# Kernel tuning notes

Measured on AMD Instinct MI355X. Metric: run time of the kernel, lower is better.

Reference implementation:

```python
import jax, jax.numpy as jnp
import numpy as np

N_NODES = 50000
N_EDGES = 800000
IN_DIM, HID_DIM, OUT_DIM = 128, 256, 64


def setup_inputs() -> dict:
    key = jax.random.key(0)
    k1, k2, k3, k4 = jax.random.split(key, 4)
    x = jax.random.normal(k1, (N_NODES, IN_DIM), dtype=jnp.float32)
    edge_index = jax.random.randint(k2, (2, N_EDGES), 0, N_NODES, dtype=jnp.int32)
    # Glorot-ish scaled weights
    W1 = jax.random.normal(k3, (IN_DIM, HID_DIM), dtype=jnp.float32) * (1.0 / np.sqrt(IN_DIM))
    W2 = jax.random.normal(k4, (HID_DIM, OUT_DIM), dtype=jnp.float32) * (1.0 / np.sqrt(HID_DIM))
    b1 = jnp.zeros((HID_DIM,), dtype=jnp.float32)
    b2 = jnp.zeros((OUT_DIM,), dtype=jnp.float32)
    return {"x": x, "edge_index": edge_index, "W1": W1, "b1": b1, "W2": W2, "b2": b2}


def _gcn_conv(x, src, dst, deg_inv_sqrt, W, b):
    # transform first (PyG GCNConv order), then edge-normalized scatter-add
    h = x @ W                                        # [N, D_out]
    norm = deg_inv_sqrt[src] * deg_inv_sqrt[dst]     # [E]
    msgs = h[src] * norm[:, None]                    # [E, D_out]
    agg = jax.ops.segment_sum(msgs, dst, num_segments=x.shape[0])
    return agg + b


def reference(x, edge_index, W1, b1, W2, b2):
    n = x.shape[0]
    loops = jnp.arange(n, dtype=edge_index.dtype)
    src = jnp.concatenate([edge_index[0], loops])    # add self-loops
    dst = jnp.concatenate([edge_index[1], loops])
    deg = jax.ops.segment_sum(jnp.ones_like(dst, dtype=x.dtype), dst, num_segments=n)
    deg_inv_sqrt = jnp.where(deg > 0, jax.lax.rsqrt(jnp.maximum(deg, 1e-12)), 0.0)
    h = jax.nn.relu(_gcn_conv(x, src, dst, deg_inv_sqrt, W1, b1))
    h = _gcn_conv(h, src, dst, deg_inv_sqrt, W2, b2)
    return jax.nn.log_softmax(h, axis=1)
```

## Files before the change

kernel.cpp:

```cpp
#include <hip/hip_runtime.h>
#include <hip/hip_bf16.h>
#include <math.h>

#define N_NODES 50000
#define N_EDGES 800000
#define IN_DIM 128
#define HID_DIM 256
#define OUT_DIM 64
#define NPART 196
#define CAP 8192
#define CHUNK 2048
#define NPB ((N_EDGES + CHUNK - 1) / CHUNK)

typedef __attribute__((ext_vector_type(8))) short bf16x8;
typedef __attribute__((ext_vector_type(4))) short short4v;
typedef __attribute__((ext_vector_type(4))) float f32x4;

__device__ inline short f2bf(float f) {
    unsigned u = __float_as_uint(f);
    unsigned r = (u + 0x7fffu + ((u >> 16) & 1u)) >> 16;
    return (short)r;
}
__device__ inline float bf_lo(unsigned u) { return __uint_as_float(u << 16); }
__device__ inline float bf_hi(unsigned u) { return __uint_as_float(u & 0xffff0000u); }

__global__ __launch_bounds__(256) void part1_pack_kernel(const int* __restrict__ src,
                                                         const int* __restrict__ dst,
                                                         int* __restrict__ coarseCursor,
                                                         uint2* __restrict__ sedge,
                                                         const float* __restrict__ W1,
                                                         const float* __restrict__ W2,
                                                         short* __restrict__ Bp1,
                                                         short* __restrict__ Bp2, int E) {
    __shared__ int cnt_l[NPART];
    __shared__ int pref[NPART];
    __shared__ int gbase[NPART];
    __shared__ int ws4[4];
    __shared__ uint2 stage[CHUNK];
    int tid = threadIdx.x;
    if (blockIdx.x >= NPB) {
        int idx = (blockIdx.x - NPB) * 256 + tid;
        const float* W; short* Bp; int N;
        const int T1 = (IN_DIM / 32) * (HID_DIM / 16) * 64;
        const int T2 = (HID_DIM / 32) * (OUT_DIM / 16) * 64;
        if (idx < T1) { W = W1; Bp = Bp1; N = HID_DIM; }
        else { idx -= T1; if (idx >= T2) return; W = W2; Bp = Bp2; N = OUT_DIM; }
        int lane = idx & 63;
        int frag = idx >> 6;
        int ntiles = N >> 4;
        int nt = frag % ntiles;
        int kt = frag / ntiles;
        int col = nt * 16 + (lane & 15);
        int krow = kt * 32 + (lane >> 4) * 8;
        bf16x8 pk;
        #pragma unroll
        for (int j = 0; j < 8; j++) pk[j] = f2bf(W[(size_t)(krow + j) * N + col]);
        *((bf16x8*)(Bp + (size_t)idx * 8)) = pk;
        return;
    }
    int e0 = blockIdx.x * CHUNK;
    if (tid < NPART) cnt_l[tid] = 0;
    __syncthreads();
    int es[CHUNK / 256], ed[CHUNK / 256];
    #pragma unroll
    for (int j = 0; j < CHUNK / 256; j++) {
        int e = e0 + j * 256 + tid;
        if (e < E) {
            es[j] = src[e]; ed[j] = dst[e];
            atomicAdd(&cnt_l[ed[j] >> 8], 1);
        } else ed[j] = -1;
    }
    __syncthreads();
    int lane = tid & 63, wid = tid >> 6;
    int v = (tid < NPART) ? cnt_l[tid] : 0;
    int s = v;
    #pragma unroll
    for (int off = 1; off < 64; off <<= 1) {
        int t = __shfl_up(s, off, 64);
        if (lane >= off) s += t;
    }
    if (lane == 63) ws4[wid] = s;
    __syncthreads();
    int wp = 0;
    #pragma unroll
    for (int w = 0; w < 4; w++) wp += (w < wid) ? ws4[w] : 0;
    int excl = s - v + wp;
    if (tid < NPART) pref[tid] = excl;
    __syncthreads();
    if (tid < NPART) cnt_l[tid] = excl;
    __syncthreads();
    #pragma unroll
    for (int j = 0; j < CHUNK / 256; j++) {
        if (ed[j] >= 0) {
            int c = ed[j] >> 8;
            int p = atomicAdd(&cnt_l[c], 1);
            stage[p] = make_uint2((unsigned)es[j], (unsigned)ed[j]);
        }
    }
    __syncthreads();
    if (tid < NPART) {
        int cl = cnt_l[tid] - pref[tid];
        gbase[tid] = (cl > 0) ? (tid * CAP + atomicAdd(&coarseCursor[tid], cl)) : 0;
    }
    __syncthreads();
    int total = (e0 + CHUNK <= E) ? CHUNK : (E - e0);
    for (int i = tid; i < total; i += 256) {
        uint2 ev = stage[i];
        int c = (int)(ev.y >> 8);
        sedge[gbase[c] + (i - pref[c])] = ev;
    }
}

__global__ __launch_bounds__(256) void part2_kernel(const uint2* __restrict__ sedge,
                                                    const int* __restrict__ coarseCnt,
                                                    int* __restrict__ offs,
                                                    int* __restrict__ cntg,
                                                    float* __restrict__ dis,
                                                    int* __restrict__ ssrc,
                                                    const float* __restrict__ x,
                                                    short* __restrict__ xb, int n) {
    __shared__ int kcnt[256];
    __shared__ int ws4[4];
    __shared__ float sdis[256];
    int b = blockIdx.x, tid = threadIdx.x;
    int base = b * CAP;
    int cb = coarseCnt[b];
    kcnt[tid] = 0;
    __syncthreads();
    for (int i = tid; i < cb; i += 256) {
        uint2 ev = sedge[base + i];
        atomicAdd(&kcnt[ev.y & 255], 1);
    }
    __syncthreads();
    int v = kcnt[tid];
    int lane = tid & 63, wid = tid >> 6;
    int s = v;
    #pragma unroll
    for (int off = 1; off < 64; off <<= 1) {
        int t = __shfl_up(s, off, 64);
        if (lane >= off) s += t;
    }
    if (lane == 63) ws4[wid] = s;
    __syncthreads();
    int wp = 0;
    #pragma unroll
    for (int w = 0; w < 4; w++) wp += (w < wid) ? ws4[w] : 0;
    int excl = s - v + wp;
    int node = b * 256 + tid;
    float dn = rsqrtf((float)v + 1.0f);
    if (node < n) {
        offs[node] = base + excl;
        cntg[node] = v;
        dis[node] = dn;
    }
    sdis[tid] = dn;
    __syncthreads();
    kcnt[tid] = base + excl;
    __syncthreads();
    for (int i = tid; i < cb; i += 256) {
        uint2 ev = sedge[base + i];
        int pos = atomicAdd(&kcnt[ev.y & 255], 1);
        ssrc[pos] = (int)ev.x;
    }
    int rlane = tid & 31, rgrp = tid >> 5;
    for (int rb = 0; rb < 32; rb++) {
        int row = rb * 8 + rgrp;
        int nd = b * 256 + row;
        if (nd >= n) break;
        float d2 = sdis[row];
        float4 vv = ((const float4*)(x + (size_t)nd * IN_DIM))[rlane];
        short4v o = {f2bf(vv.x * d2), f2bf(vv.y * d2), f2bf(vv.z * d2), f2bf(vv.w * d2)};
        *((short4v*)(xb + (size_t)nd * IN_DIM + rlane * 4)) = o;
    }
}

__global__ void agg1_kernel(const short* __restrict__ xb, const int* __restrict__ ssrc,
                            const int* __restrict__ offs, const int* __restrict__ cnt,
                            const float* __restrict__ dis, short* __restrict__ aggx, int n) {
    int lane = threadIdx.x & 63;
    int node = blockIdx.x * 4 + (threadIdx.x >> 6);
    if (node >= n) return;
    int grp = lane >> 3, l8 = lane & 7;
    int start = offs[node], c = cnt[node];
    int vidx = (lane < c) ? ssrc[start + lane] : 0;
    float acc[16] = {};
    int lim = (c < 64) ? c : 64;
    int rounds = (lim + 15) >> 4;
    for (int r = 0; r < rounds; r++) {
        int j0 = r * 16 + grp;
        int j1 = j0 + 8;
        int i0 = (j0 < 63) ? j0 : 63;
        int i1 = (j1 < 63) ? j1 : 63;
        int s0 = __shfl(vidx, i0, 64);
        int s1 = __shfl(vidx, i1, 64);
        float g0 = (j0 < lim) ? 1.0f : 0.0f;
        float g1 = (j1 < lim) ? 1.0f : 0.0f;
        const uint4* r0 = (const uint4*)(xb + (size_t)s0 * IN_DIM + l8 * 16);
        const uint4* r1 = (const uint4*)(xb + (size_t)s1 * IN_DIM + l8 * 16);
        uint4 a0 = r0[0], a1 = r0[1];
        uint4 b0 = r1[0], b1 = r1[1];
        acc[0]  += g0 * bf_lo(a0.x); acc[1]  += g0 * bf_hi(a0.x);
        acc[2]  += g0 * bf_lo(a0.y); acc[3]  += g0 * bf_hi(a0.y);
        acc[4]  += g0 * bf_lo(a0.z); acc[5]  += g0 * bf_hi(a0.z);
        acc[6]  += g0 * bf_lo(a0.w); acc[7]  += g0 * bf_hi(a0.w);
        acc[8]  += g0 * bf_lo(a1.x); acc[9]  += g0 * bf_hi(a1.x);
        acc[10] += g0 * bf_lo(a1.y); acc[11] += g0 * bf_hi(a1.y);
        acc[12] += g0 * bf_lo(a1.z); acc[13] += g0 * bf_hi(a1.z);
        acc[14] += g0 * bf_lo(a1.w); acc[15] += g0 * bf_hi(a1.w);
        acc[0]  += g1 * bf_lo(b0.x); acc[1]  += g1 * bf_hi(b0.x);
        acc[2]  += g1 * bf_lo(b0.y); acc[3]  += g1 * bf_hi(b0.y);
        acc[4]  += g1 * bf_lo(b0.z); acc[5]  += g1 * bf_hi(b0.z);
        acc[6]  += g1 * bf_lo(b0.w); acc[7]  += g1 * bf_hi(b0.w);
        acc[8]  += g1 * bf_lo(b1.x); acc[9]  += g1 * bf_hi(b1.x);
        acc[10] += g1 * bf_lo(b1.y); acc[11] += g1 * bf_hi(b1.y);
        acc[12] += g1 * bf_lo(b1.z); acc[13] += g1 * bf_hi(b1.z);
        acc[14] += g1 * bf_lo(b1.w); acc[15] += g1 * bf_hi(b1.w);
    }
    for (int j = 64 + grp; j < c; j += 8) {
        int s0 = ssrc[start + j];
        const uint4* r0 = (const uint4*)(xb + (size_t)s0 * IN_DIM + l8 * 16);
        uint4 a0 = r0[0], a1 = r0[1];
        acc[0]  += bf_lo(a0.x); acc[1]  += bf_hi(a0.x); acc[2]  += bf_lo(a0.y); acc[3]  += bf_hi(a0.y);
        acc[4]  += bf_lo(a0.z); acc[5]  += bf_hi(a0.z); acc[6]  += bf_lo(a0.w); acc[7]  += bf_hi(a0.w);
        acc[8]  += bf_lo(a1.x); acc[9]  += bf_hi(a1.x); acc[10] += bf_lo(a1.y); acc[11] += bf_hi(a1.y);
        acc[12] += bf_lo(a1.z); acc[13] += bf_hi(a1.z); acc[14] += bf_lo(a1.w); acc[15] += bf_hi(a1.w);
    }
    #pragma unroll
    for (int k = 0; k < 16; k++) {
        acc[k] += __shfl_xor(acc[k], 8, 64);
        acc[k] += __shfl_xor(acc[k], 16, 64);
        acc[k] += __shfl_xor(acc[k], 32, 64);
    }
    if (grp == 0) {
        float dn = dis[node];
        const uint4* rs = (const uint4*)(xb + (size_t)node * IN_DIM + l8 * 16);
        uint4 a0 = rs[0], a1 = rs[1];
        acc[0]  += bf_lo(a0.x); acc[1]  += bf_hi(a0.x); acc[2]  += bf_lo(a0.y); acc[3]  += bf_hi(a0.y);
        acc[4]  += bf_lo(a0.z); acc[5]  += bf_hi(a0.z); acc[6]  += bf_lo(a0.w); acc[7]  += bf_hi(a0.w);
        acc[8]  += bf_lo(a1.x); acc[9]  += bf_hi(a1.x); acc[10] += bf_lo(a1.y); acc[11] += bf_hi(a1.y);
        acc[12] += bf_lo(a1.z); acc[13] += bf_hi(a1.z); acc[14] += bf_lo(a1.w); acc[15] += bf_hi(a1.w);
        bf16x8 o0, o1;
        #pragma unroll
        for (int k = 0; k < 8; k++) { o0[k] = f2bf(acc[k] * dn); o1[k] = f2bf(acc[k + 8] * dn); }
        short* dst0 = aggx + (size_t)node * IN_DIM + l8 * 16;
        *((bf16x8*)dst0) = o0;
        *((bf16x8*)(dst0 + 8)) = o1;
    }
}

#define H1_STRIDE 264
__global__ __launch_bounds__(256) void gemm_fused_kernel(const short* __restrict__ A,
                                                         const short* __restrict__ Bp1,
                                                         const short* __restrict__ Bp2,
                                                         const float* __restrict__ b1,
                                                         const float* __restrict__ dis,
                                                         short* __restrict__ h2, int M) {
    __shared__ short lds_h1[4][16][H1_STRIDE];
    int lane = threadIdx.x & 63;
    int w = threadIdx.x >> 6;
    int rowBase = blockIdx.x * 64 + w * 16;
    int arow = rowBase + (lane & 15);
    int kseg = lane >> 4;
    int col0 = lane & 15;

    constexpr int NT1 = HID_DIM / 16;
    f32x4 acc1[NT1] = {};
    #pragma unroll
    for (int kt = 0; kt < IN_DIM / 32; kt++) {
        bf16x8 a = {};
        if (arow < M)
            a = *((const bf16x8*)(A + (size_t)arow * IN_DIM + kt * 32 + kseg * 8));
        #pragma unroll
        for (int nt = 0; nt < NT1; nt++) {
            bf16x8 b = *((const bf16x8*)(Bp1 + ((size_t)(kt * NT1 + nt) * 64 + lane) * 8));
            acc1[nt] = __builtin_amdgcn_mfma_f32_16x16x32_bf16(a, b, acc1[nt], 0, 0, 0);
        }
    }
    #pragma unroll
    for (int nt = 0; nt < NT1; nt++) {
        float bv = b1[nt * 16 + col0];
        #pragma unroll
        for (int i = 0; i < 4; i++) {
            float v = fmaxf(acc1[nt][i] + bv, 0.0f);
            lds_h1[w][kseg * 4 + i][nt * 16 + col0] = f2bf(v);
        }
    }
    constexpr int NT2 = OUT_DIM / 16;
    f32x4 acc2[NT2] = {};
    #pragma unroll
    for (int kt = 0; kt < HID_DIM / 32; kt++) {
        bf16x8 a = *((const bf16x8*)&lds_h1[w][lane & 15][kt * 32 + kseg * 8]);
        #pragma unroll
        for (int nt = 0; nt < NT2; nt++) {
            bf16x8 b = *((const bf16x8*)(Bp2 + ((size_t)(kt * NT2 + nt) * 64 + lane) * 8));
            acc2[nt] = __builtin_amdgcn_mfma_f32_16x16x32_bf16(a, b, acc2[nt], 0, 0, 0);
        }
    }
    #pragma unroll
    for (int i = 0; i < 4; i++) {
        int r = rowBase + kseg * 4 + i;
        if (r >= M) continue;
        float sc = dis[r];
        #pragma unroll
        for (int nt = 0; nt < NT2; nt++)
            h2[(size_t)r * OUT_DIM + nt * 16 + col0] = f2bf(acc2[nt][i] * sc);
    }
}

__global__ void agg2_kernel(const short* __restrict__ h2, const int* __restrict__ ssrc,
                            const int* __restrict__ offs, const int* __restrict__ cnt,
                            const float* __restrict__ dis, const float* __restrict__ b2,
                            float* __restrict__ out, int n) {
    int lane = threadIdx.x & 63;
    int node = blockIdx.x * 4 + (threadIdx.x >> 6);
    if (node >= n) return;
    int grp = lane >> 3, l8 = lane & 7;
    int start = offs[node], c = cnt[node];
    int vidx = (lane < c) ? ssrc[start + lane] : 0;
    float acc[8] = {};
    int lim = (c < 64) ? c : 64;
    int rounds = (lim + 15) >> 4;
    for (int r = 0; r < rounds; r++) {
        int j0 = r * 16 + grp;
        int j1 = j0 + 8;
        int i0 = (j0 < 63) ? j0 : 63;
        int i1 = (j1 < 63) ? j1 : 63;
        int s0 = __shfl(vidx, i0, 64);
        int s1 = __shfl(vidx, i1, 64);
        float g0 = (j0 < lim) ? 1.0f : 0.0f;
        float g1 = (j1 < lim) ? 1.0f : 0.0f;
        uint4 p0 = *((const uint4*)(h2 + (size_t)s0 * OUT_DIM + l8 * 8));
        uint4 p1 = *((const uint4*)(h2 + (size_t)s1 * OUT_DIM + l8 * 8));
        acc[0] += g0 * bf_lo(p0.x); acc[1] += g0 * bf_hi(p0.x);
        acc[2] += g0 * bf_lo(p0.y); acc[3] += g0 * bf_hi(p0.y);
        acc[4] += g0 * bf_lo(p0.z); acc[5] += g0 * bf_hi(p0.z);
        acc[6] += g0 * bf_lo(p0.w); acc[7] += g0 * bf_hi(p0.w);
        acc[0] += g1 * bf_lo(p1.x); acc[1] += g1 * bf_hi(p1.x);
        acc[2] += g1 * bf_lo(p1.y); acc[3] += g1 * bf_hi(p1.y);
        acc[4] += g1 * bf_lo(p1.z); acc[5] += g1 * bf_hi(p1.z);
        acc[6] += g1 * bf_lo(p1.w); acc[7] += g1 * bf_hi(p1.w);
    }
    for (int j = 64 + grp; j < c; j += 8) {
        int s0 = ssrc[start + j];
        uint4 p0 = *((const uint4*)(h2 + (size_t)s0 * OUT_DIM + l8 * 8));
        acc[0] += bf_lo(p0.x); acc[1] += bf_hi(p0.x); acc[2] += bf_lo(p0.y); acc[3] += bf_hi(p0.y);
        acc[4] += bf_lo(p0.z); acc[5] += bf_hi(p0.z); acc[6] += bf_lo(p0.w); acc[7] += bf_hi(p0.w);
    }
    #pragma unroll
    for (int k = 0; k < 8; k++) {
        acc[k] += __shfl_xor(acc[k], 8, 64);
        acc[k] += __shfl_xor(acc[k], 16, 64);
        acc[k] += __shfl_xor(acc[k], 32, 64);
    }
    float dn = dis[node];
    uint4 pv = *((const uint4*)(h2 + (size_t)node * OUT_DIM + l8 * 8));
    float4 bb0 = ((const float4*)b2)[l8 * 2];
    float4 bb1 = ((const float4*)b2)[l8 * 2 + 1];
    acc[0] = (acc[0] + bf_lo(pv.x)) * dn + bb0.x;
    acc[1] = (acc[1] + bf_hi(pv.x)) * dn + bb0.y;
    acc[2] = (acc[2] + bf_lo(pv.y)) * dn + bb0.z;
    acc[3] = (acc[3] + bf_hi(pv.y)) * dn + bb0.w;
    acc[4] = (acc[4] + bf_lo(pv.z)) * dn + bb1.x;
    acc[5] = (acc[5] + bf_hi(pv.z)) * dn + bb1.y;
    acc[6] = (acc[6] + bf_lo(pv.w)) * dn + bb1.z;
    acc[7] = (acc[7] + bf_hi(pv.w)) * dn + bb1.w;
    float m = acc[0];
    #pragma unroll
    for (int k = 1; k < 8; k++) m = fmaxf(m, acc[k]);
    #pragma unroll
    for (int off = 1; off < 8; off <<= 1) m = fmaxf(m, __shfl_xor(m, off, 64));
    float ex = 0.0f;
    #pragma unroll
    for (int k = 0; k < 8; k++) ex += expf(acc[k] - m);
    #pragma unroll
    for (int off = 1; off < 8; off <<= 1) ex += __shfl_xor(ex, off, 64);
    float ls = m + logf(ex);
    if (grp == 0) {
        float4 o0 = {acc[0] - ls, acc[1] - ls, acc[2] - ls, acc[3] - ls};
        float4 o1 = {acc[4] - ls, acc[5] - ls, acc[6] - ls, acc[7] - ls};
        ((float4*)(out + (size_t)node * OUT_DIM))[l8 * 2] = o0;
        ((float4*)(out + (size_t)node * OUT_DIM))[l8 * 2 + 1] = o1;
    }
}

extern "C" void kernel_launch(void* const* d_in, const int* in_sizes, int n_in,
                              void* d_out, int out_size, void* d_ws, size_t ws_size,
                              hipStream_t stream) {
    const float* x  = (const float*)d_in[0];
    const int*   ei = (const int*)d_in[1];
    const float* W1 = (const float*)d_in[2];
    const float* b1 = (const float*)d_in[3];
    const float* W2 = (const float*)d_in[4];
    const float* b2 = (const float*)d_in[5];
    float* out = (float*)d_out;
    char* ws = (char*)d_ws;

    const int* srcp = ei;
    const int* dstp = ei + N_EDGES;

    int*   coarseCursor = (int*)(ws);
    int*   offs   = (int*)(ws + 4096);
    int*   cntg   = (int*)(ws + 262144);
    float* dis    = (float*)(ws + 524288);
    short* Bp1    = (short*)(ws + 786432);
    short* Bp2    = (short*)(ws + 851968);
    int*   ssrc   = (int*)(ws + 917504);
    uint2* sedge  = (uint2*)(ws + 7340032);
    short* aggx   = (short*)(ws + 7340032);
    short* xb     = (short*)(ws + 20185088);
    short* h2     = (short*)(ws + 32985088);

    hipMemsetAsync(coarseCursor, 0, NPART * 4, stream);

    part1_pack_kernel<<<NPB + 24, 256, 0, stream>>>(srcp, dstp, coarseCursor, sedge,
                                                    W1, W2, Bp1, Bp2, N_EDGES);
    part2_kernel<<<NPART, 256, 0, stream>>>(sedge, coarseCursor, offs, cntg, dis, ssrc,
                                            x, xb, N_NODES);
    agg1_kernel<<<(N_NODES + 3) / 4, 256, 0, stream>>>(xb, ssrc, offs, cntg, dis, aggx, N_NODES);
    gemm_fused_kernel<<<(N_NODES + 63) / 64, 256, 0, stream>>>(aggx, Bp1, Bp2, b1, dis,
                                                               h2, N_NODES);
    agg2_kernel<<<(N_NODES + 3) / 4, 256, 0, stream>>>(h2, ssrc, offs, cntg, dis, b2, out, N_NODES);
}
```

Baseline: 198.0 us.

## Restructure aggregation kernels to one-feature-per-lane edge loops

```diff
diff --git a/kernel.cpp b/kernel.cpp
--- a/kernel.cpp
+++ b/kernel.cpp
@@ -174,78 +174,45 @@
     }
 }
 
-__global__ void agg1_kernel(const short* __restrict__ xb, const int* __restrict__ ssrc,
-                            const int* __restrict__ offs, const int* __restrict__ cnt,
-                            const float* __restrict__ dis, short* __restrict__ aggx, int n) {
+__global__ __launch_bounds__(256) void agg1_kernel(const short* __restrict__ xb,
+                                                   const int* __restrict__ ssrc,
+                                                   const int* __restrict__ offs,
+                                                   const int* __restrict__ cnt,
+                                                   const float* __restrict__ dis,
+                                                   short* __restrict__ aggx, int n) {
     int lane = threadIdx.x & 63;
     int node = blockIdx.x * 4 + (threadIdx.x >> 6);
     if (node >= n) return;
-    int grp = lane >> 3, l8 = lane & 7;
-    int start = offs[node], c = cnt[node];
-    int vidx = (lane < c) ? ssrc[start + lane] : 0;
-    float acc[16] = {};
-    int lim = (c < 64) ? c : 64;
-    int rounds = (lim + 15) >> 4;
-    for (int r = 0; r < rounds; r++) {
-        int j0 = r * 16 + grp;
-        int j1 = j0 + 8;
-        int i0 = (j0 < 63) ? j0 : 63;
-        int i1 = (j1 < 63) ? j1 : 63;
-        int s0 = __shfl(vidx, i0, 64);
-        int s1 = __shfl(vidx, i1, 64);
-        float g0 = (j0 < lim) ? 1.0f : 0.0f;
-        float g1 = (j1 < lim) ? 1.0f : 0.0f;
-        const uint4* r0 = (const uint4*)(xb + (size_t)s0 * IN_DIM + l8 * 16);
-        const uint4* r1 = (const uint4*)(xb + (size_t)s1 * IN_DIM + l8 * 16);
-        uint4 a0 = r0[0], a1 = r0[1];
-        uint4 b0 = r1[0], b1 = r1[1];
-        acc[0]  += g0 * bf_lo(a0.x); acc[1]  += g0 * bf_hi(a0.x);
-        acc[2]  += g0 * bf_lo(a0.y); acc[3]  += g0 * bf_hi(a0.y);
-        acc[4]  += g0 * bf_lo(a0.z); acc[5]  += g0 * bf_hi(a0.z);
-        acc[6]  += g0 * bf_lo(a0.w); acc[7]  += g0 * bf_hi(a0.w);
-        acc[8]  += g0 * bf_lo(a1.x); acc[9]  += g0 * bf_hi(a1.x);
-        acc[10] += g0 * bf_lo(a1.y); acc[11] += g0 * bf_hi(a1.y);
-        acc[12] += g0 * bf_lo(a1.z); acc[13] += g0 * bf_hi(a1.z);
-        acc[14] += g0 * bf_lo(a1.w); acc[15] += g0 * bf_hi(a1.w);
-        acc[0]  += g1 * bf_lo(b0.x); acc[1]  += g1 * bf_hi(b0.x);
-        acc[2]  += g1 * bf_lo(b0.y); acc[3]  += g1 * bf_hi(b0.y);
-        acc[4]  += g1 * bf_lo(b0.z); acc[5]  += g1 * bf_hi(b0.z);
-        acc[6]  += g1 * bf_lo(b0.w); acc[7]  += g1 * bf_hi(b0.w);
-        acc[8]  += g1 * bf_lo(b1.x); acc[9]  += g1 * bf_hi(b1.x);
-        acc[10] += g1 * bf_lo(b1.y); acc[11] += g1 * bf_hi(b1.y);
-        acc[12] += g1 * bf_lo(b1.z); acc[13] += g1 * bf_hi(b1.z);
-        acc[14] += g1 * bf_lo(b1.w); acc[15] += g1 * bf_hi(b1.w);
-    }
-    for (int j = 64 + grp; j < c; j += 8) {
-        int s0 = ssrc[start + j];
-        const uint4* r0 = (const uint4*)(xb + (size_t)s0 * IN_DIM + l8 * 16);
-        uint4 a0 = r0[0], a1 = r0[1];
-        acc[0]  += bf_lo(a0.x); acc[1]  += bf_hi(a0.x); acc[2]  += bf_lo(a0.y); acc[3]  += bf_hi(a0.y);
-        acc[4]  += bf_lo(a0.z); acc[5]  += bf_hi(a0.z); acc[6]  += bf_lo(a0.w); acc[7]  += bf_hi(a0.w);
-        acc[8]  += bf_lo(a1.x); acc[9]  += bf_hi(a1.x); acc[10] += bf_lo(a1.y); acc[11] += bf_hi(a1.y);
-        acc[12] += bf_lo(a1.z); acc[13] += bf_hi(a1.z); acc[14] += bf_lo(a1.w); acc[15] += bf_hi(a1.w);
-    }
-    #pragma unroll
-    for (int k = 0; k < 16; k++) {
-        acc[k] += __shfl_xor(acc[k], 8, 64);
-        acc[k] += __shfl_xor(acc[k], 16, 64);
-        acc[k] += __shfl_xor(acc[k], 32, 64);
-    }
-    if (grp == 0) {
-        float dn = dis[node];
-        const uint4* rs = (const uint4*)(xb + (size_t)node * IN_DIM + l8 * 16);
-        uint4 a0 = rs[0], a1 = rs[1];
-        acc[0]  += bf_lo(a0.x); acc[1]  += bf_hi(a0.x); acc[2]  += bf_lo(a0.y); acc[3]  += bf_hi(a0.y);
-        acc[4]  += bf_lo(a0.z); acc[5]  += bf_hi(a0.z); acc[6]  += bf_lo(a0.w); acc[7]  += bf_hi(a0.w);
-        acc[8]  += bf_lo(a1.x); acc[9]  += bf_hi(a1.x); acc[10] += bf_lo(a1.y); acc[11] += bf_hi(a1.y);
-        acc[12] += bf_lo(a1.z); acc[13] += bf_hi(a1.z); acc[14] += bf_lo(a1.w); acc[15] += bf_hi(a1.w);
-        bf16x8 o0, o1;
-        #pragma unroll
-        for (int k = 0; k < 8; k++) { o0[k] = f2bf(acc[k] * dn); o1[k] = f2bf(acc[k + 8] * dn); }
-        short* dst0 = aggx + (size_t)node * IN_DIM + l8 * 16;
-        *((bf16x8*)dst0) = o0;
-        *((bf16x8*)(dst0 + 8)) = o1;
-    }
+    int start = __builtin_amdgcn_readfirstlane(offs[node]);
+    int c = __builtin_amdgcn_readfirstlane(cnt[node]);
+    const unsigned* base = (const unsigned*)xb;
+    float a0 = 0.0f, a1 = 0.0f;
+    int j = 0;
+    for (; j + 4 <= c; j += 4) {
+        int i0 = ssrc[start + j];
+        int i1 = ssrc[start + j + 1];
+        int i2 = ssrc[start + j + 2];
+        int i3 = ssrc[start + j + 3];
+        unsigned u0 = base[(size_t)i0 * (IN_DIM / 2) + lane];
+        unsigned u1 = base[(size_t)i1 * (IN_DIM / 2) + lane];
+        unsigned u2 = base[(size_t)i2 * (IN_DIM / 2) + lane];
+        unsigned u3 = base[(size_t)i3 * (IN_DIM / 2) + lane];
+        a0 += bf_lo(u0); a1 += bf_hi(u0);
+        a0 += bf_lo(u1); a1 += bf_hi(u1);
+        a0 += bf_lo(u2); a1 += bf_hi(u2);
+        a0 += bf_lo(u3); a1 += bf_hi(u3);
+    }
+    for (; j < c; j++) {
+        int i0 = ssrc[start + j];
+        unsigned u0 = base[(size_t)i0 * (IN_DIM / 2) + lane];
+        a0 += bf_lo(u0); a1 += bf_hi(u0);
+    }
+    unsigned us = base[(size_t)node * (IN_DIM / 2) + lane];
+    a0 += bf_lo(us); a1 += bf_hi(us);
+    float dn = dis[node];
+    a0 *= dn; a1 *= dn;
+    unsigned o = ((unsigned)(unsigned short)f2bf(a1) << 16) | (unsigned)(unsigned short)f2bf(a0);
+    ((unsigned*)aggx)[(size_t)node * (IN_DIM / 2) + lane] = o;
 }
 
 #define H1_STRIDE 264
@@ -307,80 +274,51 @@
     }
 }
 
-__global__ void agg2_kernel(const short* __restrict__ h2, const int* __restrict__ ssrc,
-                            const int* __restrict__ offs, const int* __restrict__ cnt,
-                            const float* __restrict__ dis, const float* __restrict__ b2,
-                            float* __restrict__ out, int n) {
+__global__ __launch_bounds__(256) void agg2_kernel(const short* __restrict__ h2,
+                                                   const int* __restrict__ ssrc,
+                                                   const int* __restrict__ offs,
+                                                   const int* __restrict__ cnt,
+                                                   const float* __restrict__ dis,
+                                                   const float* __restrict__ b2,
+                                                   float* __restrict__ out, int n) {
     int lane = threadIdx.x & 63;
     int node = blockIdx.x * 4 + (threadIdx.x >> 6);
     if (node >= n) return;
-    int grp = lane >> 3, l8 = lane & 7;
-    int start = offs[node], c = cnt[node];
-    int vidx = (lane < c) ? ssrc[start + lane] : 0;
-    float acc[8] = {};
-    int lim = (c < 64) ? c : 64;
-    int rounds = (lim + 15) >> 4;
-    for (int r = 0; r < rounds; r++) {
-        int j0 = r * 16 + grp;
-        int j1 = j0 + 8;
-        int i0 = (j0 < 63) ? j0 : 63;
-        int i1 = (j1 < 63) ? j1 : 63;
-        int s0 = __shfl(vidx, i0, 64);
-        int s1 = __shfl(vidx, i1, 64);
-        float g0 = (j0 < lim) ? 1.0f : 0.0f;
-        float g1 = (j1 < lim) ? 1.0f : 0.0f;
-        uint4 p0 = *((const uint4*)(h2 + (size_t)s0 * OUT_DIM + l8 * 8));
-        uint4 p1 = *((const uint4*)(h2 + (size_t)s1 * OUT_DIM + l8 * 8));
-        acc[0] += g0 * bf_lo(p0.x); acc[1] += g0 * bf_hi(p0.x);
-        acc[2] += g0 * bf_lo(p0.y); acc[3] += g0 * bf_hi(p0.y);
-        acc[4] += g0 * bf_lo(p0.z); acc[5] += g0 * bf_hi(p0.z);
-        acc[6] += g0 * bf_lo(p0.w); acc[7] += g0 * bf_hi(p0.w);
-        acc[0] += g1 * bf_lo(p1.x); acc[1] += g1 * bf_hi(p1.x);
-        acc[2] += g1 * bf_lo(p1.y); acc[3] += g1 * bf_hi(p1.y);
-        acc[4] += g1 * bf_lo(p1.z); acc[5] += g1 * bf_hi(p1.z);
-        acc[6] += g1 * bf_lo(p1.w); acc[7] += g1 * bf_hi(p1.w);
-    }
-    for (int j = 64 + grp; j < c; j += 8) {
-        int s0 = ssrc[start + j];
-        uint4 p0 = *((const uint4*)(h2 + (size_t)s0 * OUT_DIM + l8 * 8));
-        acc[0] += bf_lo(p0.x); acc[1] += bf_hi(p0.x); acc[2] += bf_lo(p0.y); acc[3] += bf_hi(p0.y);
-        acc[4] += bf_lo(p0.z); acc[5] += bf_hi(p0.z); acc[6] += bf_lo(p0.w); acc[7] += bf_hi(p0.w);
-    }
-    #pragma unroll
-    for (int k = 0; k < 8; k++) {
-        acc[k] += __shfl_xor(acc[k], 8, 64);
-        acc[k] += __shfl_xor(acc[k], 16, 64);
-        acc[k] += __shfl_xor(acc[k], 32, 64);
-    }
+    int start = __builtin_amdgcn_readfirstlane(offs[node]);
+    int c = __builtin_amdgcn_readfirstlane(cnt[node]);
+    const unsigned short* base = (const unsigned short*)h2;
+    float a = 0.0f;
+    int j = 0;
+    for (; j + 4 <= c; j += 4) {
+        int i0 = ssrc[start + j];
+        int i1 = ssrc[start + j + 1];
+        int i2 = ssrc[start + j + 2];
+        int i3 = ssrc[start + j + 3];
+        unsigned short u0 = base[(size_t)i0 * OUT_DIM + lane];
+        unsigned short u1 = base[(size_t)i1 * OUT_DIM + lane];
+        unsigned short u2 = base[(size_t)i2 * OUT_DIM + lane];
+        unsigned short u3 = base[(size_t)i3 * OUT_DIM + lane];
+        a += __uint_as_float((unsigned)u0 << 16);
+        a += __uint_as_float((unsigned)u1 << 16);
+        a += __uint_as_float((unsigned)u2 << 16);
+        a += __uint_as_float((unsigned)u3 << 16);
+    }
+    for (; j < c; j++) {
+        int i0 = ssrc[start + j];
+        unsigned short u0 = base[(size_t)i0 * OUT_DIM + lane];
+        a += __uint_as_float((unsigned)u0 << 16);
+    }
+    unsigned short us = base[(size_t)node * OUT_DIM + lane];
     float dn = dis[node];
-    uint4 pv = *((const uint4*)(h2 + (size_t)node * OUT_DIM + l8 * 8));
-    float4 bb0 = ((const float4*)b2)[l8 * 2];
-    float4 bb1 = ((const float4*)b2)[l8 * 2 + 1];
-    acc[0] = (acc[0] + bf_lo(pv.x)) * dn + bb0.x;
-    acc[1] = (acc[1] + bf_hi(pv.x)) * dn + bb0.y;
-    acc[2] = (acc[2] + bf_lo(pv.y)) * dn + bb0.z;
-    acc[3] = (acc[3] + bf_hi(pv.y)) * dn + bb0.w;
-    acc[4] = (acc[4] + bf_lo(pv.z)) * dn + bb1.x;
-    acc[5] = (acc[5] + bf_hi(pv.z)) * dn + bb1.y;
-    acc[6] = (acc[6] + bf_lo(pv.w)) * dn + bb1.z;
-    acc[7] = (acc[7] + bf_hi(pv.w)) * dn + bb1.w;
-    float m = acc[0];
-    #pragma unroll
-    for (int k = 1; k < 8; k++) m = fmaxf(m, acc[k]);
-    #pragma unroll
-    for (int off = 1; off < 8; off <<= 1) m = fmaxf(m, __shfl_xor(m, off, 64));
-    float ex = 0.0f;
-    #pragma unroll
-    for (int k = 0; k < 8; k++) ex += expf(acc[k] - m);
-    #pragma unroll
-    for (int off = 1; off < 8; off <<= 1) ex += __shfl_xor(ex, off, 64);
-    float ls = m + logf(ex);
-    if (grp == 0) {
-        float4 o0 = {acc[0] - ls, acc[1] - ls, acc[2] - ls, acc[3] - ls};
-        float4 o1 = {acc[4] - ls, acc[5] - ls, acc[6] - ls, acc[7] - ls};
-        ((float4*)(out + (size_t)node * OUT_DIM))[l8 * 2] = o0;
-        ((float4*)(out + (size_t)node * OUT_DIM))[l8 * 2 + 1] = o1;
-    }
+    a = (a + __uint_as_float((unsigned)us << 16)) * dn + b2[lane];
+    float m = a;
+    #pragma unroll
+    for (int off = 1; off < 64; off <<= 1) m = fmaxf(m, __shfl_xor(m, off, 64));
+    float e = expf(a - m);
+    float sum = e;
+    #pragma unroll
+    for (int off = 1; off < 64; off <<= 1) sum += __shfl_xor(sum, off, 64);
+    out[(size_t)node * OUT_DIM + lane] = a - m - logf(sum);
 }
 
 extern "C" void kernel_launch(void* const* d_in, const int* in_sizes, int n_in,
```

Measured after the change: 205.8 us. 1.04x slower.

## Move x bf16 conversion into part1 and count per-node degrees with global atomics

Applied to the files above, without the earlier changes.

```diff
diff --git a/kernel.cpp b/kernel.cpp
--- a/kernel.cpp
+++ b/kernel.cpp
@@ -11,6 +11,8 @@
 #define CAP 8192
 #define CHUNK 2048
 #define NPB ((N_EDGES + CHUNK - 1) / CHUNK)
+#define NPACK 24
+#define NPREP NPART
 
 typedef __attribute__((ext_vector_type(8))) short bf16x8;
 typedef __attribute__((ext_vector_type(4))) short short4v;
@@ -24,20 +26,36 @@
 __device__ inline float bf_lo(unsigned u) { return __uint_as_float(u << 16); }
 __device__ inline float bf_hi(unsigned u) { return __uint_as_float(u & 0xffff0000u); }
 
-__global__ __launch_bounds__(256) void part1_pack_kernel(const int* __restrict__ src,
-                                                         const int* __restrict__ dst,
-                                                         int* __restrict__ coarseCursor,
-                                                         uint2* __restrict__ sedge,
-                                                         const float* __restrict__ W1,
-                                                         const float* __restrict__ W2,
-                                                         short* __restrict__ Bp1,
-                                                         short* __restrict__ Bp2, int E) {
+__global__ __launch_bounds__(256) void part1_pack_prep_kernel(const int* __restrict__ src,
+                                                              const int* __restrict__ dst,
+                                                              int* __restrict__ coarseCursor,
+                                                              int* __restrict__ cntg,
+                                                              uint2* __restrict__ sedge,
+                                                              const float* __restrict__ W1,
+                                                              const float* __restrict__ W2,
+                                                              short* __restrict__ Bp1,
+                                                              short* __restrict__ Bp2,
+                                                              const float* __restrict__ x,
+                                                              short* __restrict__ xb, int E) {
     __shared__ int cnt_l[NPART];
     __shared__ int pref[NPART];
     __shared__ int gbase[NPART];
     __shared__ int ws4[4];
     __shared__ uint2 stage[CHUNK];
     int tid = threadIdx.x;
+    if (blockIdx.x >= NPB + NPACK) {
+        int pb = blockIdx.x - NPB - NPACK;
+        int rlane = tid & 31, rgrp = tid >> 5;
+        for (int rb = 0; rb < 32; rb++) {
+            int row = rb * 8 + rgrp;
+            int nd = pb * 256 + row;
+            if (nd >= N_NODES) break;
+            float4 vv = ((const float4*)(x + (size_t)nd * IN_DIM))[rlane];
+            short4v o = {f2bf(vv.x), f2bf(vv.y), f2bf(vv.z), f2bf(vv.w)};
+            *((short4v*)(xb + (size_t)nd * IN_DIM + rlane * 4)) = o;
+        }
+        return;
+    }
     if (blockIdx.x >= NPB) {
         int idx = (blockIdx.x - NPB) * 256 + tid;
         const float* W; short* Bp; int N;
@@ -68,6 +86,7 @@
         if (e < E) {
             es[j] = src[e]; ed[j] = dst[e];
             atomicAdd(&cnt_l[ed[j] >> 8], 1);
+            atomicAdd(&cntg[ed[j]], 1);
         } else ed[j] = -1;
     }
     __syncthreads();
@@ -113,26 +132,17 @@
 
 __global__ __launch_bounds__(256) void part2_kernel(const uint2* __restrict__ sedge,
                                                     const int* __restrict__ coarseCnt,
+                                                    const int* __restrict__ cntg,
                                                     int* __restrict__ offs,
-                                                    int* __restrict__ cntg,
                                                     float* __restrict__ dis,
-                                                    int* __restrict__ ssrc,
-                                                    const float* __restrict__ x,
-                                                    short* __restrict__ xb, int n) {
+                                                    int* __restrict__ ssrc, int n) {
     __shared__ int kcnt[256];
     __shared__ int ws4[4];
-    __shared__ float sdis[256];
     int b = blockIdx.x, tid = threadIdx.x;
     int base = b * CAP;
     int cb = coarseCnt[b];
-    kcnt[tid] = 0;
-    __syncthreads();
-    for (int i = tid; i < cb; i += 256) {
-        uint2 ev = sedge[base + i];
-        atomicAdd(&kcnt[ev.y & 255], 1);
-    }
-    __syncthreads();
-    int v = kcnt[tid];
+    int nd = b * 256 + tid;
+    int v = (nd < n) ? cntg[nd] : 0;
     int lane = tid & 63, wid = tid >> 6;
     int s = v;
     #pragma unroll
@@ -146,31 +156,16 @@
     #pragma unroll
     for (int w = 0; w < 4; w++) wp += (w < wid) ? ws4[w] : 0;
     int excl = s - v + wp;
-    int node = b * 256 + tid;
-    float dn = rsqrtf((float)v + 1.0f);
-    if (node < n) {
-        offs[node] = base + excl;
-        cntg[node] = v;
-        dis[node] = dn;
-    }
-    sdis[tid] = dn;
-    __syncthreads();
+    if (nd < n) {
+        offs[nd] = base + excl;
+        dis[nd] = rsqrtf((float)v + 1.0f);
+    }
     kcnt[tid] = base + excl;
     __syncthreads();
     for (int i = tid; i < cb; i += 256) {
         uint2 ev = sedge[base + i];
         int pos = atomicAdd(&kcnt[ev.y & 255], 1);
         ssrc[pos] = (int)ev.x;
-    }
-    int rlane = tid & 31, rgrp = tid >> 5;
-    for (int rb = 0; rb < 32; rb++) {
-        int row = rb * 8 + rgrp;
-        int nd = b * 256 + row;
-        if (nd >= n) break;
-        float d2 = sdis[row];
-        float4 vv = ((const float4*)(x + (size_t)nd * IN_DIM))[rlane];
-        short4v o = {f2bf(vv.x * d2), f2bf(vv.y * d2), f2bf(vv.z * d2), f2bf(vv.w * d2)};
-        *((short4v*)(xb + (size_t)nd * IN_DIM + rlane * 4)) = o;
     }
 }
 
@@ -193,8 +188,8 @@
         int i1 = (j1 < 63) ? j1 : 63;
         int s0 = __shfl(vidx, i0, 64);
         int s1 = __shfl(vidx, i1, 64);
-        float g0 = (j0 < lim) ? 1.0f : 0.0f;
-        float g1 = (j1 < lim) ? 1.0f : 0.0f;
+        float g0 = (j0 < lim) ? dis[s0] : 0.0f;
+        float g1 = (j1 < lim) ? dis[s1] : 0.0f;
         const uint4* r0 = (const uint4*)(xb + (size_t)s0 * IN_DIM + l8 * 16);
         const uint4* r1 = (const uint4*)(xb + (size_t)s1 * IN_DIM + l8 * 16);
         uint4 a0 = r0[0], a1 = r0[1];
@@ -218,12 +213,17 @@
     }
     for (int j = 64 + grp; j < c; j += 8) {
         int s0 = ssrc[start + j];
+        float w0 = dis[s0];
         const uint4* r0 = (const uint4*)(xb + (size_t)s0 * IN_DIM + l8 * 16);
         uint4 a0 = r0[0], a1 = r0[1];
-        acc[0]  += bf_lo(a0.x); acc[1]  += bf_hi(a0.x); acc[2]  += bf_lo(a0.y); acc[3]  += bf_hi(a0.y);
-        acc[4]  += bf_lo(a0.z); acc[5]  += bf_hi(a0.z); acc[6]  += bf_lo(a0.w); acc[7]  += bf_hi(a0.w);
-        acc[8]  += bf_lo(a1.x); acc[9]  += bf_hi(a1.x); acc[10] += bf_lo(a1.y); acc[11] += bf_hi(a1.y);
-        acc[12] += bf_lo(a1.z); acc[13] += bf_hi(a1.z); acc[14] += bf_lo(a1.w); acc[15] += bf_hi(a1.w);
+        acc[0]  += w0 * bf_lo(a0.x); acc[1]  += w0 * bf_hi(a0.x);
+        acc[2]  += w0 * bf_lo(a0.y); acc[3]  += w0 * bf_hi(a0.y);
+        acc[4]  += w0 * bf_lo(a0.z); acc[5]  += w0 * bf_hi(a0.z);
+        acc[6]  += w0 * bf_lo(a0.w); acc[7]  += w0 * bf_hi(a0.w);
+        acc[8]  += w0 * bf_lo(a1.x); acc[9]  += w0 * bf_hi(a1.x);
+        acc[10] += w0 * bf_lo(a1.y); acc[11] += w0 * bf_hi(a1.y);
+        acc[12] += w0 * bf_lo(a1.z); acc[13] += w0 * bf_hi(a1.z);
+        acc[14] += w0 * bf_lo(a1.w); acc[15] += w0 * bf_hi(a1.w);
     }
     #pragma unroll
     for (int k = 0; k < 16; k++) {
@@ -235,10 +235,14 @@
         float dn = dis[node];
         const uint4* rs = (const uint4*)(xb + (size_t)node * IN_DIM + l8 * 16);
         uint4 a0 = rs[0], a1 = rs[1];
-        acc[0]  += bf_lo(a0.x); acc[1]  += bf_hi(a0.x); acc[2]  += bf_lo(a0.y); acc[3]  += bf_hi(a0.y);
-        acc[4]  += bf_lo(a0.z); acc[5]  += bf_hi(a0.z); acc[6]  += bf_lo(a0.w); acc[7]  += bf_hi(a0.w);
-        acc[8]  += bf_lo(a1.x); acc[9]  += bf_hi(a1.x); acc[10] += bf_lo(a1.y); acc[11] += bf_hi(a1.y);
-        acc[12] += bf_lo(a1.z); acc[13] += bf_hi(a1.z); acc[14] += bf_lo(a1.w); acc[15] += bf_hi(a1.w);
+        acc[0]  += dn * bf_lo(a0.x); acc[1]  += dn * bf_hi(a0.x);
+        acc[2]  += dn * bf_lo(a0.y); acc[3]  += dn * bf_hi(a0.y);
+        acc[4]  += dn * bf_lo(a0.z); acc[5]  += dn * bf_hi(a0.z);
+        acc[6]  += dn * bf_lo(a0.w); acc[7]  += dn * bf_hi(a0.w);
+        acc[8]  += dn * bf_lo(a1.x); acc[9]  += dn * bf_hi(a1.x);
+        acc[10] += dn * bf_lo(a1.y); acc[11] += dn * bf_hi(a1.y);
+        acc[12] += dn * bf_lo(a1.z); acc[13] += dn * bf_hi(a1.z);
+        acc[14] += dn * bf_lo(a1.w); acc[15] += dn * bf_hi(a1.w);
         bf16x8 o0, o1;
         #pragma unroll
         for (int k = 0; k < 8; k++) { o0[k] = f2bf(acc[k] * dn); o1[k] = f2bf(acc[k + 8] * dn); }
@@ -399,23 +403,22 @@
     const int* dstp = ei + N_EDGES;
 
     int*   coarseCursor = (int*)(ws);
-    int*   offs   = (int*)(ws + 4096);
-    int*   cntg   = (int*)(ws + 262144);
-    float* dis    = (float*)(ws + 524288);
-    short* Bp1    = (short*)(ws + 786432);
-    short* Bp2    = (short*)(ws + 851968);
-    int*   ssrc   = (int*)(ws + 917504);
-    uint2* sedge  = (uint2*)(ws + 7340032);
-    short* aggx   = (short*)(ws + 7340032);
-    short* xb     = (short*)(ws + 20185088);
-    short* h2     = (short*)(ws + 32985088);
-
-    hipMemsetAsync(coarseCursor, 0, NPART * 4, stream);
-
-    part1_pack_kernel<<<NPB + 24, 256, 0, stream>>>(srcp, dstp, coarseCursor, sedge,
-                                                    W1, W2, Bp1, Bp2, N_EDGES);
-    part2_kernel<<<NPART, 256, 0, stream>>>(sedge, coarseCursor, offs, cntg, dis, ssrc,
-                                            x, xb, N_NODES);
+    int*   cntg   = (int*)(ws + 1024);
+    int*   offs   = (int*)(ws + 204800);
+    float* dis    = (float*)(ws + 409600);
+    short* Bp1    = (short*)(ws + 614400);
+    short* Bp2    = (short*)(ws + 679936);
+    int*   ssrc   = (int*)(ws + 720896);
+    uint2* sedge  = (uint2*)(ws + 7143424);
+    short* aggx   = (short*)(ws + 7143424);
+    short* xb     = (short*)(ws + 19988480);
+    short* h2     = (short*)(ws + 32788480);
+
+    hipMemsetAsync(ws, 0, 1024 + N_NODES * 4, stream);
+
+    part1_pack_prep_kernel<<<NPB + NPACK + NPREP, 256, 0, stream>>>(
+        srcp, dstp, coarseCursor, cntg, sedge, W1, W2, Bp1, Bp2, x, xb, N_EDGES);
+    part2_kernel<<<NPART, 256, 0, stream>>>(sedge, coarseCursor, cntg, offs, dis, ssrc, N_NODES);
     agg1_kernel<<<(N_NODES + 3) / 4, 256, 0, stream>>>(xb, ssrc, offs, cntg, dis, aggx, N_NODES);
     gemm_fused_kernel<<<(N_NODES + 63) / 64, 256, 0, stream>>>(aggx, Bp1, Bp2, b1, dis,
                                                                h2, N_NODES);
```

After: 218.6 us. 10.4% more time.
